# Kernel tuning notes

Hardware: AMD Instinct MI355X
Metric: run time of the kernel (lower is better)

Reference implementation:

```python
import jax, jax.numpy as jnp
import numpy as np

WEIGHT_BITS = 8
INPUT_BITS = 8
HIDDEN = 4096
INTERMEDIATE = 16384
CLIP_INIT = 2.5


def _sym_quantize(x, clip_val, num_bits):
    """Symmetric layerwise uniform quantization with STE (PACT-style clip).

    Forward: clamp to [-clip, clip], round to 2^(b-1)-1 levels, dequantize.
    """
    clip_val = jnp.abs(clip_val)
    x_c = jnp.clip(x, -clip_val, clip_val)
    scale = clip_val / (2 ** (num_bits - 1) - 1)
    q = jnp.round(x_c / scale) * scale
    # straight-through estimator: gradient flows through the clamp only
    return x_c + jax.lax.stop_gradient(q - x_c)


def setup_inputs() -> dict:
    key = jax.random.key(0)
    k1, k2, k3 = jax.random.split(key, 3)
    hidden_states = jax.random.normal(k1, (2, 2048, HIDDEN), dtype=jnp.float32)
    # nn.Linear default init scale ~ 1/sqrt(fan_in)
    weight = jax.random.normal(k2, (INTERMEDIATE, HIDDEN), dtype=jnp.float32) / np.sqrt(HIDDEN)
    bias = jax.random.normal(k3, (INTERMEDIATE,), dtype=jnp.float32) * 0.01
    weight_clip_val = jnp.float32(CLIP_INIT)
    input_clip_val = jnp.float32(CLIP_INIT)
    return {
        "hidden_states": hidden_states,
        "weight": weight,
        "bias": bias,
        "weight_clip_val": weight_clip_val,
        "input_clip_val": input_clip_val,
    }


def reference(hidden_states, weight, bias, weight_clip_val, input_clip_val):
    wq = _sym_quantize(weight, weight_clip_val, WEIGHT_BITS)        # [I, H]
    xq = _sym_quantize(hidden_states, input_clip_val, INPUT_BITS)   # [B, S, H]
    out = jnp.einsum("bsh,ih->bsi", xq, wq) + bias                  # [B, S, I]
    return jax.nn.relu(out)
```

## Files before the change

### kernel.cpp

```cpp
#include <hip/hip_runtime.h>


#define HIDDEN 4096
#define INTER 16384
#define MDIM 4096
#define BK 128
#define NT (HIDDEN / BK)

typedef int v4i __attribute__((ext_vector_type(4)));

__global__ __launch_bounds__(256) void quantize_kernel(
    const float* __restrict__ x,
    signed char* __restrict__ q,
    const float* __restrict__ clip_ptr,
    int n4)
{
    int i = blockIdx.x * blockDim.x + threadIdx.x;
    if (i >= n4) return;
    float c = fabsf(clip_ptr[0]);
    float inv_scale = 127.0f / c;
    float4 v = reinterpret_cast<const float4*>(x)[i];
    int q0 = __float2int_rn(fminf(fmaxf(v.x, -c), c) * inv_scale);
    int q1 = __float2int_rn(fminf(fmaxf(v.y, -c), c) * inv_scale);
    int q2 = __float2int_rn(fminf(fmaxf(v.z, -c), c) * inv_scale);
    int q3 = __float2int_rn(fminf(fmaxf(v.w, -c), c) * inv_scale);
    int pack = (q0 & 0xff) | ((q1 & 0xff) << 8) | ((q2 & 0xff) << 16) | (q3 << 24);
    reinterpret_cast<int*>(q)[i] = pack;
}


#define GLL(src, dst) __builtin_amdgcn_global_load_lds( \
    (const __attribute__((address_space(1))) void*)(src), \
    (__attribute__((address_space(3))) void*)(dst), 16, 0, 0)

#define STAGE(gptr, lptr) do { \
    GLL((gptr), (lptr)); \
    GLL((gptr) + (size_t)64 * HIDDEN, (lptr) + 8192); } while (0)

#define BARX() __builtin_amdgcn_s_barrier()
#define LGKM0() asm volatile("s_waitcnt lgkmcnt(0)" ::: "memory")
#define VM6() asm volatile("s_waitcnt vmcnt(6)" ::: "memory")
#define VM4() asm volatile("s_waitcnt vmcnt(4)" ::: "memory")
#define VM0() asm volatile("s_waitcnt vmcnt(0)" ::: "memory")
#define VMNOP()
#define PRIO1() __builtin_amdgcn_s_setprio(1)
#define PRIO0() __builtin_amdgcn_s_setprio(0)

#define READ_A(cb, qm) do { _Pragma("unroll") \
    for (int m_ = 0; m_ < 4; m_++) { \
      const signed char* p_ = &As[cb][(qm) * 16384 + aOff + m_ * 2048]; \
      a[m_][0] = *reinterpret_cast<const v4i*>(p_ + c0); \
      a[m_][1] = *reinterpret_cast<const v4i*>(p_ + c1); } } while (0)

#define READ_B(cb, qn) do { _Pragma("unroll") \
    for (int n_ = 0; n_ < 2; n_++) { \
      const signed char* p_ = &Bs[cb][(qn) * 16384 + bOff + n_ * 2048]; \
      b[n_][0] = *reinterpret_cast<const v4i*>(p_ + c0); \
      b[n_][1] = *reinterpret_cast<const v4i*>(p_ + c1); } } while (0)

#define MFMA_Q(qm, qn) do { _Pragma("unroll") \
    for (int m_ = 0; m_ < 4; m_++) { _Pragma("unroll") \
      for (int n_ = 0; n_ < 2; n_++) { \
        acc[qm][qn][m_][n_] = __builtin_amdgcn_mfma_i32_16x16x64_i8( \
            a[m_][0], b[n_][0], acc[qm][qn][m_][n_], 0, 0, 0); \
        acc[qm][qn][m_][n_] = __builtin_amdgcn_mfma_i32_16x16x64_i8( \
            a[m_][1], b[n_][1], acc[qm][qn][m_][n_], 0, 0, 0); } } } while (0)

#define GROUP(cb, ob, T, SN, S2, VMW) do { \
     \
    READ_A(cb, 0); READ_B(cb, 0); \
    if (SN) STAGE(gB + (size_t)((T) + 1) * BK, &Bs[ob][0] + ldsT); \
    BARX(); LGKM0(); PRIO1(); MFMA_Q(0, 0); PRIO0(); BARX(); \
     \
    READ_B(cb, 1); \
    if (S2) STAGE(gA + (size_t)((T) + 2) * BK, &As[cb][0] + ldsT); \
    BARX(); LGKM0(); PRIO1(); MFMA_Q(0, 1); PRIO0(); BARX(); \
     \
    READ_A(cb, 1); \
    if (S2) STAGE(gB + (size_t)128 * HIDDEN + (size_t)((T) + 2) * BK, &Bs[cb][16384] + ldsT); \
    BARX(); LGKM0(); PRIO1(); MFMA_Q(1, 1); PRIO0(); BARX(); \
     \
    READ_B(cb, 0); \
    if (S2) STAGE(gA + (size_t)128 * HIDDEN + (size_t)((T) + 2) * BK, &As[cb][16384] + ldsT); \
    VMW(); \
    BARX(); LGKM0(); PRIO1(); MFMA_Q(1, 0); PRIO0(); BARX(); \
  } while (0)

__global__ __launch_bounds__(512, 2) void gemm_i8_kernel(
    const signed char* __restrict__ qA,
    const signed char* __restrict__ qB,
    const float* __restrict__ bias,
    const float* __restrict__ wclip,
    const float* __restrict__ iclip,
    float* __restrict__ out)
{
    __shared__ __align__(16) signed char As[2][32768];
    __shared__ __align__(16) signed char Bs[2][32768];

    const int t = threadIdx.x;
    const int L = t & 63;
    const int W = t >> 6;
    const int wm = W >> 2;
    const int wn = W & 3;
    const int lane16 = L & 15;
    const int quad = L >> 4;
    const int swz = lane16 & 7;

    int wg = blockIdx.y * 64 + blockIdx.x;
    wg = (wg & 7) * 128 + (wg >> 3);
    const int mBase = (wg >> 6) * 256;
    const int nBase = (wg & 63) * 256;

    const int sRow = t >> 3;
    const int sColSwz = ((t & 7) ^ (sRow & 7)) * 16;
    const signed char* gA = qA + (size_t)(mBase + sRow) * HIDDEN + sColSwz;
    const signed char* gB = qB + (size_t)(nBase + sRow) * HIDDEN + sColSwz;
    const int ldsT = t * 16;

    const int aOff = (wm * 64 + lane16) * 128;
    const int bOff = (wn * 32 + lane16) * 128;
    const int c0 = (quad ^ swz) * 16;
    const int c1 = ((quad + 4) ^ swz) * 16;

    v4i acc[2][2][4][2];
#pragma unroll
    for (int i = 0; i < 2; i++)
#pragma unroll
        for (int j = 0; j < 2; j++)
#pragma unroll
            for (int m = 0; m < 4; m++)
#pragma unroll
                for (int n = 0; n < 2; n++)
                    acc[i][j][m][n] = (v4i){0, 0, 0, 0};

    v4i a[4][2], b[2][2];

    STAGE(gA, &As[0][0] + ldsT);
    STAGE(gB, &Bs[0][0] + ldsT);
    STAGE(gA + (size_t)128 * HIDDEN, &As[0][16384] + ldsT);
    STAGE(gB + (size_t)128 * HIDDEN, &Bs[0][16384] + ldsT);
    VM4();
    STAGE(gA + BK, &As[1][0] + ldsT);
    STAGE(gB + (size_t)128 * HIDDEN + BK, &Bs[1][16384] + ldsT);
    STAGE(gA + (size_t)128 * HIDDEN + BK, &As[1][16384] + ldsT);
    VM6();
    BARX();

    for (int T = 0; T < NT - 2; T += 2) {
        GROUP(0, 1, T,     1, 1, VM6);
        GROUP(1, 0, T + 1, 1, 1, VM6);
    }
    GROUP(0, 1, NT - 2, 1, 0, VM0);
    GROUP(1, 0, NT - 1, 0, 0, VMNOP);

    const float scale = (fabsf(wclip[0]) / 127.0f) * (fabsf(iclip[0]) / 127.0f);

    float bv[2][2];
#pragma unroll
    for (int qn = 0; qn < 2; qn++)
#pragma unroll
        for (int n = 0; n < 2; n++)
            bv[qn][n] = bias[nBase + qn * 128 + wn * 32 + n * 16 + lane16];

#pragma unroll
    for (int qm = 0; qm < 2; qm++)
#pragma unroll
        for (int m = 0; m < 4; m++)
#pragma unroll
            for (int r = 0; r < 4; r++) {
                const int row = mBase + qm * 128 + wm * 64 + m * 16 + quad * 4 + r;
                float* orow = out + (size_t)row * INTER + nBase + wn * 32 + lane16;
#pragma unroll
                for (int qn = 0; qn < 2; qn++)
#pragma unroll
                    for (int n = 0; n < 2; n++) {
                        float v = (float)acc[qm][qn][m][n][r] * scale + bv[qn][n];
                        orow[qn * 128 + n * 16] = fmaxf(v, 0.0f);
                    }
            }
}

extern "C" void kernel_launch(void* const* d_in, const int* in_sizes, int n_in,
                              void* d_out, int out_size, void* d_ws, size_t ws_size,
                              hipStream_t stream) {
    const float* hidden_states  = (const float*)d_in[0];
    const float* weight         = (const float*)d_in[1];
    const float* bias           = (const float*)d_in[2];
    const float* weight_clip    = (const float*)d_in[3];
    const float* input_clip     = (const float*)d_in[4];
    float* out = (float*)d_out;

    signed char* qA = (signed char*)d_ws;
    signed char* qB = qA + (size_t)MDIM * HIDDEN;

    {
        int n4 = MDIM * HIDDEN / 4;
        quantize_kernel<<<n4 / 256, 256, 0, stream>>>(hidden_states, qA, input_clip, n4);
    }
    {
        int n4 = INTER * HIDDEN / 4;
        quantize_kernel<<<n4 / 256, 256, 0, stream>>>(weight, qB, weight_clip, n4);
    }

    dim3 grid(INTER / 256, MDIM / 256);
    gemm_i8_kernel<<<grid, 512, 0, stream>>>(qA, qB, bias, weight_clip, input_clip, out);
}
```

Baseline: 735.5 us.

## Pre-pack B in MFMA fragment layout and load it straight to registers

The weight quantize kernel now writes int8 weights in a tiled layout that matches the MFMA B-fragment order. The GEMM reads B fragments directly from global memory into registers, double-buffered as b0/b1, so B no longer goes through LDS and its shared buffers are removed. The goal is to cut LDS traffic and barriers for B and to free LDS. The cost is that every wave issues its own global loads for B, with less reuse across waves in the block, and the prefetch distance and vmcnt bookkeeping change.

```diff
diff --git a/kernel.cpp b/kernel.cpp
--- a/kernel.cpp
+++ b/kernel.cpp
@@ -28,6 +28,30 @@
     reinterpret_cast<int*>(q)[i] = pack;
 }
 
+__global__ __launch_bounds__(256) void quantize_pack_b_kernel(
+    const float* __restrict__ x,
+    signed char* __restrict__ qp,
+    const float* __restrict__ clip_ptr,
+    int n4)
+{
+    int i = blockIdx.x * blockDim.x + threadIdx.x;
+    if (i >= n4) return;
+    float c = fabsf(clip_ptr[0]);
+    float inv_scale = 127.0f / c;
+    float4 v = reinterpret_cast<const float4*>(x)[i];
+    int q0 = __float2int_rn(fminf(fmaxf(v.x, -c), c) * inv_scale);
+    int q1 = __float2int_rn(fminf(fmaxf(v.y, -c), c) * inv_scale);
+    int q2 = __float2int_rn(fminf(fmaxf(v.z, -c), c) * inv_scale);
+    int q3 = __float2int_rn(fminf(fmaxf(v.w, -c), c) * inv_scale);
+    int pack = (q0 & 0xff) | ((q1 & 0xff) << 8) | ((q2 & 0xff) << 16) | (q3 << 24);
+    int n = i >> 10;
+    int k = (i & 1023) << 2;
+    size_t addr = ((size_t)(n >> 4) << 16) | ((size_t)(k >> 6) << 10)
+                | ((size_t)((k >> 4) & 3) << 8) | ((size_t)(n & 15) << 4)
+                | (size_t)(k & 15);
+    *reinterpret_cast<int*>(qp + addr) = pack;
+}
+
 
 #define GLL(src, dst) __builtin_amdgcn_global_load_lds( \
     (const __attribute__((address_space(1))) void*)(src), \
@@ -39,9 +63,8 @@
 
 #define BARX() __builtin_amdgcn_s_barrier()
 #define LGKM0() asm volatile("s_waitcnt lgkmcnt(0)" ::: "memory")
-#define VM6() asm volatile("s_waitcnt vmcnt(6)" ::: "memory")
-#define VM4() asm volatile("s_waitcnt vmcnt(4)" ::: "memory")
-#define VM0() asm volatile("s_waitcnt vmcnt(0)" ::: "memory")
+#define VM12() asm volatile("s_waitcnt vmcnt(12)" ::: "memory")
+#define VM8() asm volatile("s_waitcnt vmcnt(8)" ::: "memory")
 #define VMNOP()
 #define PRIO1() __builtin_amdgcn_s_setprio(1)
 #define PRIO0() __builtin_amdgcn_s_setprio(0)
@@ -52,50 +75,52 @@
       a[m_][0] = *reinterpret_cast<const v4i*>(p_ + c0); \
       a[m_][1] = *reinterpret_cast<const v4i*>(p_ + c1); } } while (0)
 
-#define READ_B(cb, qn) do { _Pragma("unroll") \
-    for (int n_ = 0; n_ < 2; n_++) { \
-      const signed char* p_ = &Bs[cb][(qn) * 16384 + bOff + n_ * 2048]; \
-      b[n_][0] = *reinterpret_cast<const v4i*>(p_ + c0); \
-      b[n_][1] = *reinterpret_cast<const v4i*>(p_ + c1); } } while (0)
-
-#define MFMA_Q(qm, qn) do { _Pragma("unroll") \
+#define LOADB(dst, qn, kf0) do { _Pragma("unroll") \
+    for (int n_ = 0; n_ < 2; n_++) { _Pragma("unroll") \
+      for (int kk_ = 0; kk_ < 2; kk_++) { \
+        dst[n_][kk_] = *reinterpret_cast<const v4i*>( \
+            bpw + (((size_t)((qn) * 8 + n_) << 16) | \
+                   ((size_t)((kf0) + kk_) << 10)) + L16); } } } while (0)
+
+#define MFMA_Q(qm, qn, bset) do { _Pragma("unroll") \
     for (int m_ = 0; m_ < 4; m_++) { _Pragma("unroll") \
-      for (int n_ = 0; n_ < 2; n_++) { \
+      for (int n_ = 0; n_ < 2; n_++) \
         acc[qm][qn][m_][n_] = __builtin_amdgcn_mfma_i32_16x16x64_i8( \
-            a[m_][0], b[n_][0], acc[qm][qn][m_][n_], 0, 0, 0); \
+            a[m_][0], bset[n_][0], acc[qm][qn][m_][n_], 0, 0, 0); } \
+    _Pragma("unroll") \
+    for (int m_ = 0; m_ < 4; m_++) { _Pragma("unroll") \
+      for (int n_ = 0; n_ < 2; n_++) \
         acc[qm][qn][m_][n_] = __builtin_amdgcn_mfma_i32_16x16x64_i8( \
-            a[m_][1], b[n_][1], acc[qm][qn][m_][n_], 0, 0, 0); } } } while (0)
-
-#define GROUP(cb, ob, T, SN, S2, VMW) do { \
-     \
-    READ_A(cb, 0); READ_B(cb, 0); \
-    if (SN) STAGE(gB + (size_t)((T) + 1) * BK, &Bs[ob][0] + ldsT); \
-    BARX(); LGKM0(); PRIO1(); MFMA_Q(0, 0); PRIO0(); BARX(); \
-     \
-    READ_B(cb, 1); \
+            a[m_][1], bset[n_][1], acc[qm][qn][m_][n_], 0, 0, 0); } } while (0)
+
+#define GROUP(cb, T, S2, SB, VMW) do { \
+     \
+    READ_A(cb, 0); \
+    LOADB(b1, 1, (T) * 2); \
+    BARX(); LGKM0(); PRIO1(); MFMA_Q(0, 0, b0); PRIO0(); BARX(); \
+     \
     if (S2) STAGE(gA + (size_t)((T) + 2) * BK, &As[cb][0] + ldsT); \
-    BARX(); LGKM0(); PRIO1(); MFMA_Q(0, 1); PRIO0(); BARX(); \
+    BARX(); PRIO1(); MFMA_Q(0, 1, b1); PRIO0(); BARX(); \
      \
     READ_A(cb, 1); \
-    if (S2) STAGE(gB + (size_t)128 * HIDDEN + (size_t)((T) + 2) * BK, &Bs[cb][16384] + ldsT); \
-    BARX(); LGKM0(); PRIO1(); MFMA_Q(1, 1); PRIO0(); BARX(); \
-     \
-    READ_B(cb, 0); \
-    if (S2) STAGE(gA + (size_t)128 * HIDDEN + (size_t)((T) + 2) * BK, &As[cb][16384] + ldsT); \
+    BARX(); LGKM0(); PRIO1(); MFMA_Q(1, 0, b0); PRIO0(); BARX(); \
+     \
+    if (SB) LOADB(b0, 0, ((T) + 1) * 2); \
+    if (S2) STAGE(gA + (size_t)128 * HIDDEN + (size_t)((T) + 2) * BK, \
+                  &As[cb][16384] + ldsT); \
     VMW(); \
-    BARX(); LGKM0(); PRIO1(); MFMA_Q(1, 0); PRIO0(); BARX(); \
+    BARX(); PRIO1(); MFMA_Q(1, 1, b1); PRIO0(); BARX(); \
   } while (0)
 
 __global__ __launch_bounds__(512, 2) void gemm_i8_kernel(
     const signed char* __restrict__ qA,
-    const signed char* __restrict__ qB,
+    const signed char* __restrict__ Bp,
     const float* __restrict__ bias,
     const float* __restrict__ wclip,
     const float* __restrict__ iclip,
     float* __restrict__ out)
 {
     __shared__ __align__(16) signed char As[2][32768];
-    __shared__ __align__(16) signed char Bs[2][32768];
 
     const int t = threadIdx.x;
     const int L = t & 63;
@@ -105,6 +130,7 @@
     const int lane16 = L & 15;
     const int quad = L >> 4;
     const int swz = lane16 & 7;
+    const int L16 = L * 16;
 
     int wg = blockIdx.y * 64 + blockIdx.x;
     wg = (wg & 7) * 128 + (wg >> 3);
@@ -114,14 +140,14 @@
     const int sRow = t >> 3;
     const int sColSwz = ((t & 7) ^ (sRow & 7)) * 16;
     const signed char* gA = qA + (size_t)(mBase + sRow) * HIDDEN + sColSwz;
-    const signed char* gB = qB + (size_t)(nBase + sRow) * HIDDEN + sColSwz;
     const int ldsT = t * 16;
 
     const int aOff = (wm * 64 + lane16) * 128;
-    const int bOff = (wn * 32 + lane16) * 128;
     const int c0 = (quad ^ swz) * 16;
     const int c1 = ((quad + 4) ^ swz) * 16;
 
+    const signed char* bpw = Bp + ((size_t)((nBase >> 4) + wn * 2) << 16);
+
     v4i acc[2][2][4][2];
 #pragma unroll
     for (int i = 0; i < 2; i++)
@@ -133,25 +159,22 @@
                 for (int n = 0; n < 2; n++)
                     acc[i][j][m][n] = (v4i){0, 0, 0, 0};
 
-    v4i a[4][2], b[2][2];
+    v4i a[4][2], b0[2][2], b1[2][2];
 
     STAGE(gA, &As[0][0] + ldsT);
-    STAGE(gB, &Bs[0][0] + ldsT);
     STAGE(gA + (size_t)128 * HIDDEN, &As[0][16384] + ldsT);
-    STAGE(gB + (size_t)128 * HIDDEN, &Bs[0][16384] + ldsT);
-    VM4();
     STAGE(gA + BK, &As[1][0] + ldsT);
-    STAGE(gB + (size_t)128 * HIDDEN + BK, &Bs[1][16384] + ldsT);
     STAGE(gA + (size_t)128 * HIDDEN + BK, &As[1][16384] + ldsT);
-    VM6();
+    LOADB(b0, 0, 0);
+    VM8();
     BARX();
 
     for (int T = 0; T < NT - 2; T += 2) {
-        GROUP(0, 1, T,     1, 1, VM6);
-        GROUP(1, 0, T + 1, 1, 1, VM6);
+        GROUP(0, T,     1, 1, VM12);
+        GROUP(1, T + 1, 1, 1, VM12);
     }
-    GROUP(0, 1, NT - 2, 1, 0, VM0);
-    GROUP(1, 0, NT - 1, 0, 0, VMNOP);
+    GROUP(0, NT - 2, 0, 1, VM8);
+    GROUP(1, NT - 1, 0, 0, VMNOP);
 
     const float scale = (fabsf(wclip[0]) / 127.0f) * (fabsf(iclip[0]) / 127.0f);
 
@@ -191,7 +214,7 @@
     float* out = (float*)d_out;
 
     signed char* qA = (signed char*)d_ws;
-    signed char* qB = qA + (size_t)MDIM * HIDDEN;
+    signed char* Bp = qA + (size_t)MDIM * HIDDEN;
 
     {
         int n4 = MDIM * HIDDEN / 4;
@@ -199,9 +222,9 @@
     }
     {
         int n4 = INTER * HIDDEN / 4;
-        quantize_kernel<<<n4 / 256, 256, 0, stream>>>(weight, qB, weight_clip, n4);
+        quantize_pack_b_kernel<<<n4 / 256, 256, 0, stream>>>(weight, Bp, weight_clip, n4);
     }
 
     dim3 grid(INTER / 256, MDIM / 256);
-    gemm_i8_kernel<<<grid, 512, 0, stream>>>(qA, qB, bias, weight_clip, input_clip, out);
-}
+    gemm_i8_kernel<<<grid, 512, 0, stream>>>(qA, Bp, bias, weight_clip, input_clip, out);
+}
```

New measurement: 752.7 us. +2.3%, slower.
